# Kernel tuning notes

Measured on AMD Instinct MI355X. Metric: run time of the kernel, lower is better.

Reference implementation:

```python
import jax, jax.numpy as jnp
import numpy as np
import math

B, N, D, O, H = 8, 1024, 512, 512, 8
HD = O // H  # head_dim = 64


def setup_inputs() -> dict:
    key = jax.random.key(0)
    ks = jax.random.split(key, 12)
    x = jax.random.normal(ks[0], (B, N, D), dtype=jnp.float32)
    adj = jax.random.uniform(ks[1], (B, N, N), dtype=jnp.float32)  # unused by forward math
    mask = jax.random.randint(ks[2], (B, N), 0, 2) > 0  # bool padding mask
    # learned params (torch nn.Linear: y = x @ W.T + b)
    qkv_w = jax.random.normal(ks[3], (3 * O, D), dtype=jnp.float32) / math.sqrt(D)
    qkv_b = jnp.zeros((3 * O,), dtype=jnp.float32)
    # self_loop_W: 1/head_dim + U(0,1), per head, non-trainable
    self_loop_W = (1.0 / HD + jax.random.uniform(ks[4], (1, H, 1, 1))).astype(jnp.float32)
    w1 = jax.random.normal(ks[5], (O, O), dtype=jnp.float32) / math.sqrt(O)
    b1 = jnp.zeros((O,), dtype=jnp.float32)
    w2 = jax.random.normal(ks[6], (O, O), dtype=jnp.float32) / math.sqrt(O)
    b2 = jnp.zeros((O,), dtype=jnp.float32)
    wr = jax.random.normal(ks[7], (O, D), dtype=jnp.float32) / math.sqrt(D)
    br = jnp.zeros((O,), dtype=jnp.float32)
    return {"x": x, "adj": adj, "mask": mask, "self_loop_W": self_loop_W,
            "qkv_w": qkv_w, "qkv_b": qkv_b, "w1": w1, "b1": b1,
            "w2": w2, "b2": b2, "wr": wr, "br": br}


def reference(x, adj, mask, self_loop_W, qkv_w, qkv_b, w1, b1, w2, b2, wr, br):
    fmask = mask.astype(x.dtype)  # [B,N]
    # --- MoireAttention ---
    qkv = x @ qkv_w.T + qkv_b                       # [B,N,3O]
    qkv = qkv.reshape(B, N, 3, H, HD).transpose(2, 0, 3, 1, 4)  # [3,B,H,N,hd]
    Q, K, V = qkv[0], qkv[1], qkv[2]
    scores = jnp.einsum('bhnd,bhmd->bhnm', Q, K) / math.sqrt(HD)  # [B,H,N,N]
    eye = jnp.eye(N, dtype=scores.dtype)
    scores = scores + eye[None, None] * self_loop_W  # per-head diagonal self-loop bias
    mask2d = mask[:, None, :, None] & mask[:, None, None, :]  # [B,1,N,N]
    scores = jnp.where(mask2d, scores, jnp.asarray(-1e6, scores.dtype))
    attn = jax.nn.softmax(scores, axis=-1)
    h = jnp.einsum('bhnm,bhmd->bhnd', attn, V)      # [B,H,N,hd]
    h = h.transpose(0, 2, 1, 3).reshape(B, N, O)
    # --- mask, FFN (eval mode: noise/dropout are identity), mask ---
    h = h * fmask[..., None]
    h = jax.nn.relu(h @ w1.T + b1) @ w2.T + b2
    h = h * fmask[..., None]
    # --- residual blend ---
    x_proj = x @ wr.T + br
    return h * 0.5 + x_proj * 0.5
```

## Files before the change

### kernel.cpp

```cpp
#include <hip/hip_runtime.h>
#include <hip/hip_bf16.h>

typedef __attribute__((ext_vector_type(8))) short short8;
typedef __attribute__((ext_vector_type(4))) float f32x4;
typedef __attribute__((ext_vector_type(4))) short short4v;

#define BB 8
#define NN 1024
#define DD 512
#define OO 512
#define HH 8
#define HD 64
#define MM (BB * NN)

#define QSC 0.18033688f
#define KSHIFT -11.54156032f
#define KMASKED -30000.0f

__device__ __forceinline__ void gload_lds16(const void* g, void* l) {
  __builtin_amdgcn_global_load_lds(
      (const __attribute__((address_space(1))) void*)g,
      (__attribute__((address_space(3))) void*)l, 16, 0, 0);
}

__device__ __forceinline__ uint2 cvt4(float4 v) {
  union { uint2 u; __hip_bfloat16 h[4]; } t;
  t.h[0] = __float2bfloat16(v.x);
  t.h[1] = __float2bfloat16(v.y);
  t.h[2] = __float2bfloat16(v.z);
  t.h[3] = __float2bfloat16(v.w);
  return t.u;
}

#define SEG_N 10
struct ConvArgs {
  const float* src[SEG_N];
  __hip_bfloat16* dst[SEG_N];
  int n4[SEG_N];
};

__global__ void convert_kernel(ConvArgs a) {
  const int t = blockIdx.y;
  const int n4 = a.n4[t];
  const float4* fs = (const float4*)a.src[t];
  uint2* d = (uint2*)a.dst[t];
  for (int i = blockIdx.x * blockDim.x + threadIdx.x; i < n4;
       i += gridDim.x * blockDim.x)
    d[i] = cvt4(fs[i]);
}

__global__ __launch_bounds__(256) void gemm_qkv(
    const __hip_bfloat16* __restrict__ A0, const __hip_bfloat16* __restrict__ B0,
    const __hip_bfloat16* __restrict__ bias0, const __hip_bfloat16* __restrict__ bias1,
    __hip_bfloat16* __restrict__ out0, __hip_bfloat16* __restrict__ out1,
    __hip_bfloat16* __restrict__ out2, float* __restrict__ outf, int Kd) {
  __shared__ __align__(16) __hip_bfloat16 smem[16384];

  const int tid  = threadIdx.x;
  const int wave = tid >> 6;
  const int lane = tid & 63;
  const int fl   = lane & 15;
  const int fk   = (lane >> 4) * 8;
  const int wm   = (wave & 1) * 64;
  const int wn   = (wave >> 1) * 64;
  const int bid     = blockIdx.x;
  const int rowpart = 8 * (bid & 7) + ((bid >> 3) & 7);
  const int colpart = bid >> 6;
  const int m0 = rowpart * 128;
  const int n0 = colpart * 128;
  const int glr  = lane >> 2;
  const int glc  = (lane & 3) * 8;

  f32x4 acc[4][4];
#pragma unroll
  for (int i = 0; i < 4; ++i)
#pragma unroll
    for (int j = 0; j < 4; ++j) acc[i][j] = (f32x4){0.f, 0.f, 0.f, 0.f};

  char* lb = (char*)smem;
  for (int k0 = 0; k0 < Kd; k0 += 64) {
    __syncthreads();
    gload_lds16(A0 + (size_t)(m0 + wave * 16 + glr) * Kd + k0 + glc,
                lb + wave * 1024 + lane * 16);
    gload_lds16(A0 + (size_t)(m0 + 64 + wave * 16 + glr) * Kd + k0 + glc,
                lb + (wave + 4) * 1024 + lane * 16);
    gload_lds16(A0 + (size_t)(m0 + wave * 16 + glr) * Kd + k0 + 32 + glc,
                lb + 8192 + wave * 1024 + lane * 16);
    gload_lds16(A0 + (size_t)(m0 + 64 + wave * 16 + glr) * Kd + k0 + 32 + glc,
                lb + 8192 + (wave + 4) * 1024 + lane * 16);
    gload_lds16(B0 + (size_t)(n0 + wave * 16 + glr) * Kd + k0 + glc,
                lb + 16384 + wave * 1024 + lane * 16);
    gload_lds16(B0 + (size_t)(n0 + 64 + wave * 16 + glr) * Kd + k0 + glc,
                lb + 16384 + (wave + 4) * 1024 + lane * 16);
    gload_lds16(B0 + (size_t)(n0 + wave * 16 + glr) * Kd + k0 + 32 + glc,
                lb + 24576 + wave * 1024 + lane * 16);
    gload_lds16(B0 + (size_t)(n0 + 64 + wave * 16 + glr) * Kd + k0 + 32 + glc,
                lb + 24576 + (wave + 4) * 1024 + lane * 16);
    __syncthreads();

#pragma unroll
    for (int kh = 0; kh < 2; ++kh) {
      const __hip_bfloat16* Ap = smem + kh * 4096;
      const __hip_bfloat16* Bp = smem + 8192 + kh * 4096;
      short8 af[4], bfr[4];
#pragma unroll
      for (int i = 0; i < 4; ++i)
        af[i] = *(const short8*)&Ap[(wm + i * 16 + fl) * 32 + fk];
#pragma unroll
      for (int j = 0; j < 4; ++j)
        bfr[j] = *(const short8*)&Bp[(wn + j * 16 + fl) * 32 + fk];
#pragma unroll
      for (int i = 0; i < 4; ++i)
#pragma unroll
        for (int j = 0; j < 4; ++j)
          acc[i][j] = __builtin_amdgcn_mfma_f32_16x16x32_bf16(af[i], bfr[j],
                                                              acc[i][j], 0, 0, 0);
    }
  }

  const int rb = (lane >> 4) * 4;
  const int part = n0 >> 9;
  if (part < 2) {
    __hip_bfloat16* dst = (part == 0) ? out0 : out1;
    const float scf = (part == 0) ? QSC : 1.0f;
#pragma unroll
    for (int j = 0; j < 4; ++j) {
      const int colb  = n0 + wn + j * 16;
      const int o     = colb & 511;
      const int headq = o >> 6;
      const int d     = (o & 63) + fl;
      const float bi  = __bfloat162float(bias0[colb + fl]);
#pragma unroll
      for (int i = 0; i < 4; ++i) {
#pragma unroll
        for (int r = 0; r < 4; ++r) {
          const int row = m0 + wm + i * 16 + rb + r;
          const int bb  = row >> 10;
          const int nn  = row & 1023;
          dst[((size_t)((bb << 3) + headq) * NN + nn) * HD + d] =
              __float2bfloat16((acc[i][j][r] + bi) * scf);
        }
      }
    }
  } else if (part == 2) {
    __syncthreads();
    __hip_bfloat16* tsc = smem + wave * 1120;
    const int bb  = (m0 + wm) >> 10;
    const int nnb = (m0 + wm) & 1023;
    const int dl  = lane >> 2;
    const int cc  = (lane & 3) * 16;
#pragma unroll
    for (int j = 0; j < 4; ++j) {
      const int colb  = n0 + wn + j * 16;
      const int o     = colb & 511;
      const int headq = o >> 6;
      const int dbase = o & 63;
      const float bi  = __bfloat162float(bias0[colb + fl]);
#pragma unroll
      for (int i = 0; i < 4; ++i) {
#pragma unroll
        for (int r = 0; r < 4; ++r) {
          const int rr = i * 16 + rb + r;
          tsc[fl * 70 + rr] = __float2bfloat16(acc[i][j][r] + bi);
        }
      }
      uint4 r0 = *(const uint4*)&tsc[dl * 70 + cc];
      uint4 r1 = *(const uint4*)&tsc[dl * 70 + cc + 8];
      __hip_bfloat16* vdst =
          out2 + ((size_t)((bb << 3) + headq) * HD + dbase + dl) * NN + nnb;
      *(uint4*)&vdst[cc] = r0;
      *(uint4*)&vdst[cc + 8] = r1;
    }
  } else {
#pragma unroll
    for (int j = 0; j < 4; ++j) {
      const int colb = n0 + wn + j * 16;
      const int o    = colb & 511;
      const float bi = 0.5f * __bfloat162float(bias1[o + fl]);
#pragma unroll
      for (int i = 0; i < 4; ++i) {
#pragma unroll
        for (int r = 0; r < 4; ++r) {
          const int row = m0 + wm + i * 16 + rb + r;
          outf[(size_t)row * OO + o + fl] = 0.5f * acc[i][j][r] + bi;
        }
      }
    }
  }
}

__global__ __launch_bounds__(1024) void ffn_fused(
    const __hip_bfloat16* __restrict__ hb,
    const __hip_bfloat16* __restrict__ w1, const __hip_bfloat16* __restrict__ w2,
    const __hip_bfloat16* __restrict__ b1, const __hip_bfloat16* __restrict__ b2,
    const int* __restrict__ mask, float* __restrict__ outf) {
  __shared__ __align__(16) __hip_bfloat16 h1s[32 * 520];
  __shared__ float Mrow[32];

  const int tid  = threadIdx.x;
  const int wv   = tid >> 6;
  const int lane = tid & 63;
  const int fl   = lane & 15;
  const int quad = lane >> 4;
  const int fk   = quad * 8;
  const int m0   = blockIdx.x * 32;

  {
    const int col = (tid & 63) * 8;
#pragma unroll
    for (int c = 0; c < 2; ++c) {
      const int row = c * 16 + (tid >> 6);
      *(uint4*)&h1s[row * 520 + col] =
          *(const uint4*)&hb[(size_t)(m0 + row) * OO + col];
    }
    if (tid < 32) Mrow[tid] = (mask[m0 + tid] != 0) ? 1.f : 0.f;
  }
  __syncthreads();

  f32x4 acc[2][2];

  auto run_phase = [&](const __hip_bfloat16* __restrict__ W) {
    const __hip_bfloat16* wl0 = W + (size_t)(wv * 32 + fl) * 512 + fk;
    short8 a[6][2];
#pragma unroll
    for (int d = 0; d < 6; ++d)
#pragma unroll
      for (int j = 0; j < 2; ++j)
        a[d][j] = *(const short8*)(wl0 + d * 32 + j * 8192);
#pragma unroll
    for (int k = 0; k < 16; ++k) {
      short8 bh_[2];
#pragma unroll
      for (int i = 0; i < 2; ++i)
        bh_[i] = *(const short8*)&h1s[(i * 16 + fl) * 520 + k * 32 + fk];
      __builtin_amdgcn_s_setprio(1);
#pragma unroll
      for (int j = 0; j < 2; ++j)
#pragma unroll
        for (int i = 0; i < 2; ++i)
          acc[i][j] = __builtin_amdgcn_mfma_f32_16x16x32_bf16(a[k % 6][j], bh_[i],
                                                              acc[i][j], 0, 0, 0);
      __builtin_amdgcn_s_setprio(0);
      if (k < 10) {
#pragma unroll
        for (int j = 0; j < 2; ++j)
          a[k % 6][j] = *(const short8*)(wl0 + (k + 6) * 32 + j * 8192);
      }
      __builtin_amdgcn_sched_barrier(0);
    }
  };

#pragma unroll
  for (int i = 0; i < 2; ++i)
#pragma unroll
    for (int j = 0; j < 2; ++j) acc[i][j] = (f32x4){0.f, 0.f, 0.f, 0.f};
  run_phase(w1);
  __syncthreads();

#pragma unroll
  for (int j = 0; j < 2; ++j) {
    const int c0 = wv * 32 + j * 16 + quad * 4;
    union { short4v s; __hip_bfloat16 h[4]; } bv;
    bv.s = *(const short4v*)&b1[c0];
#pragma unroll
    for (int i = 0; i < 2; ++i) {
      const float mr = Mrow[i * 16 + fl];
      union { short4v s; __hip_bfloat16 h[4]; } pu;
#pragma unroll
      for (int e = 0; e < 4; ++e) {
        const float v = fmaxf(acc[i][j][e] + __bfloat162float(bv.h[e]), 0.f) * mr;
        pu.h[e] = __float2bfloat16(v);
      }
      *(short4v*)&h1s[(i * 16 + fl) * 520 + c0] = pu.s;
    }
  }
  __syncthreads();

#pragma unroll
  for (int i = 0; i < 2; ++i)
#pragma unroll
    for (int j = 0; j < 2; ++j) acc[i][j] = (f32x4){0.f, 0.f, 0.f, 0.f};
  run_phase(w2);

#pragma unroll
  for (int j = 0; j < 2; ++j) {
    const int c0 = wv * 32 + j * 16 + quad * 4;
    union { short4v s; __hip_bfloat16 h[4]; } b2v;
    b2v.s = *(const short4v*)&b2[c0];
#pragma unroll
    for (int i = 0; i < 2; ++i) {
      const float mr = Mrow[i * 16 + fl];
      const int row = m0 + i * 16 + fl;
      float4 prev = *(const float4*)&outf[(size_t)row * OO + c0];
      float4 o;
      o.x = prev.x + 0.5f * (acc[i][j][0] + mr * __bfloat162float(b2v.h[0]));
      o.y = prev.y + 0.5f * (acc[i][j][1] + mr * __bfloat162float(b2v.h[1]));
      o.z = prev.z + 0.5f * (acc[i][j][2] + mr * __bfloat162float(b2v.h[2]));
      o.w = prev.w + 0.5f * (acc[i][j][3] + mr * __bfloat162float(b2v.h[3]));
      *(float4*)&outf[(size_t)row * OO + c0] = o;
    }
  }
}

__global__ __launch_bounds__(512) void attn_kernel(
    const __hip_bfloat16* __restrict__ Qb, const __hip_bfloat16* __restrict__ Kb,
    const __hip_bfloat16* __restrict__ Vt, const __hip_bfloat16* __restrict__ slw,
    const int* __restrict__ mask, __hip_bfloat16* __restrict__ hb) {
  __shared__ __align__(16) __hip_bfloat16 QPs[256 * 72];
  __shared__ __align__(16) __hip_bfloat16 Ks[2][64 * 72];
  __shared__ __align__(16) __hip_bfloat16 Vs[2][64 * 72];
  __shared__ float Msf[NN];

  const int tid  = threadIdx.x;
  const int wave = tid >> 6;
  const int lane = tid & 63;
  const int fl   = lane & 15;
  const int quad = lane >> 4;
  const int fk   = quad * 8;
  const int rb   = quad * 4;
  const int bh   = blockIdx.x & 63;
  const int qblk = blockIdx.x >> 6;
  const int b    = bh >> 3;
  const int head = bh & 7;
  const int q0   = qblk * 256;

  const float slwL2 = __bfloat162float(slw[head]) * 1.44269504f;

  const int twf  = 2 * wave;
  const int kbdA = 4 * qblk + (twf >> 2);
  const int jdA  = twf & 3;
  const int kbdB = 4 * qblk + ((twf + 1) >> 2);
  const int jdB  = (twf + 1) & 3;

  const int srow2 = tid >> 3;
  const int sc2   = (tid & 7) * 8;
  const __hip_bfloat16* kgb = Kb + (size_t)bh * NN * HD;
  const __hip_bfloat16* vgb = Vt + (size_t)bh * HD * NN;

  uint4 kr = *(const uint4*)(kgb + (size_t)srow2 * HD + sc2);
  uint4 vr = *(const uint4*)(vgb + (size_t)srow2 * NN + sc2);
  {
    const int qr = tid >> 1;
    const int qc = (tid & 1) * 32;
    const __hip_bfloat16* qg = Qb + ((size_t)bh * NN + q0 + qr) * HD + qc;
    uint4 v0 = *(const uint4*)(qg);
    uint4 v1 = *(const uint4*)(qg + 8);
    uint4 v2 = *(const uint4*)(qg + 16);
    uint4 v3 = *(const uint4*)(qg + 24);
    *(uint4*)&QPs[qr * 72 + qc] = v0;
    *(uint4*)&QPs[qr * 72 + qc + 8] = v1;
    *(uint4*)&QPs[qr * 72 + qc + 16] = v2;
    *(uint4*)&QPs[qr * 72 + qc + 24] = v3;
#pragma unroll
    for (int k = 0; k < 2; ++k) {
      const int idx = tid * 2 + k;
      Msf[idx] = (mask[b * NN + idx] != 0) ? KSHIFT : KMASKED;
    }
  }
  *(uint4*)&Ks[0][srow2 * 72 + sc2] = kr;
  *(uint4*)&Vs[0][srow2 * 72 + sc2] = vr;
  kr = *(const uint4*)(kgb + (size_t)(64 + srow2) * HD + sc2);
  vr = *(const uint4*)(vgb + (size_t)srow2 * NN + 64 + sc2);
  __syncthreads();
  const short8 qa0A = *(const short8*)&QPs[(wave * 32 + fl) * 72 + fk];
  const short8 qa1A = *(const short8*)&QPs[(wave * 32 + fl) * 72 + fk + 32];
  const short8 qa0B = *(const short8*)&QPs[(wave * 32 + 16 + fl) * 72 + fk];
  const short8 qa1B = *(const short8*)&QPs[(wave * 32 + 16 + fl) * 72 + fk + 32];

  float lsumA = 0.f, lsumB = 0.f;
  f32x4 OaccA[4], OaccB[4];
#pragma unroll
  for (int t = 0; t < 4; ++t) {
    OaccA[t] = (f32x4){0.f, 0.f, 0.f, 0.f};
    OaccB[t] = (f32x4){0.f, 0.f, 0.f, 0.f};
  }

  for (int kb = 0; kb < NN / 64; ++kb) {
    const int kbase = kb * 64;
    const int cur   = kb & 1;
    const __hip_bfloat16* Kc = Ks[cur];
    const __hip_bfloat16* Vc = Vs[cur];

    f32x4 sfrA[4], sfrB[4];
    __builtin_amdgcn_s_setprio(1);
#pragma unroll
    for (int j = 0; j < 4; ++j) {
      const short8 kf0 = *(const short8*)&Kc[(j * 16 + fl) * 72 + fk];
      const short8 kf1 = *(const short8*)&Kc[(j * 16 + fl) * 72 + fk + 32];
      f32x4 zA = (f32x4){0.f, 0.f, 0.f, 0.f};
      zA = __builtin_amdgcn_mfma_f32_16x16x32_bf16(kf0, qa0A, zA, 0, 0, 0);
      zA = __builtin_amdgcn_mfma_f32_16x16x32_bf16(kf1, qa1A, zA, 0, 0, 0);
      sfrA[j] = zA;
      f32x4 zB = (f32x4){0.f, 0.f, 0.f, 0.f};
      zB = __builtin_amdgcn_mfma_f32_16x16x32_bf16(kf0, qa0B, zB, 0, 0, 0);
      zB = __builtin_amdgcn_mfma_f32_16x16x32_bf16(kf1, qa1B, zB, 0, 0, 0);
      sfrB[j] = zB;
    }
    __builtin_amdgcn_s_setprio(0);

    if ((fl >> 2) == quad && (kb == kbdA || kb == kbdB)) {
#pragma unroll
      for (int j = 0; j < 4; ++j)
#pragma unroll
        for (int e = 0; e < 4; ++e)
          if ((fl & 3) == e) {
            if (kb == kbdA && j == jdA) sfrA[j][e] += slwL2;
            if (kb == kbdB && j == jdB) sfrB[j][e] += slwL2;
          }
    }

#pragma unroll
    for (int j = 0; j < 4; ++j) {
      const f32x4 mb4 = *(const f32x4*)&Msf[kbase + j * 16 + quad * 4];
      union { short4v s; __hip_bfloat16 h[4]; } puA, puB;
      float psA = 0.f, psB = 0.f;
#pragma unroll
      for (int e = 0; e < 4; ++e) {
        const float pvA = exp2f(sfrA[j][e] + mb4[e]);
        psA += pvA;
        puA.h[e] = __float2bfloat16(pvA);
        const float pvB = exp2f(sfrB[j][e] + mb4[e]);
        psB += pvB;
        puB.h[e] = __float2bfloat16(pvB);
      }
      lsumA += psA;
      lsumB += psB;
      *(short4v*)&QPs[(wave * 32 + fl) * 72 + j * 16 + quad * 4] = puA.s;
      *(short4v*)&QPs[(wave * 32 + 16 + fl) * 72 + j * 16 + quad * 4] = puB.s;
    }

    const short8 paA0 = *(const short8*)&QPs[(wave * 32 + fl) * 72 + fk];
    const short8 paA1 = *(const short8*)&QPs[(wave * 32 + fl) * 72 + fk + 32];
    const short8 paB0 = *(const short8*)&QPs[(wave * 32 + 16 + fl) * 72 + fk];
    const short8 paB1 = *(const short8*)&QPs[(wave * 32 + 16 + fl) * 72 + fk + 32];
    __builtin_amdgcn_s_setprio(1);
#pragma unroll
    for (int t = 0; t < 4; ++t) {
      const short8 vf0 = *(const short8*)&Vc[(t * 16 + fl) * 72 + fk];
      const short8 vf1 = *(const short8*)&Vc[(t * 16 + fl) * 72 + fk + 32];
      OaccA[t] = __builtin_amdgcn_mfma_f32_16x16x32_bf16(paA0, vf0, OaccA[t], 0, 0, 0);
      OaccA[t] = __builtin_amdgcn_mfma_f32_16x16x32_bf16(paA1, vf1, OaccA[t], 0, 0, 0);
      OaccB[t] = __builtin_amdgcn_mfma_f32_16x16x32_bf16(paB0, vf0, OaccB[t], 0, 0, 0);
      OaccB[t] = __builtin_amdgcn_mfma_f32_16x16x32_bf16(paB1, vf1, OaccB[t], 0, 0, 0);
    }
    __builtin_amdgcn_s_setprio(0);

    if (kb + 1 < NN / 64) {
      *(uint4*)&Ks[cur ^ 1][srow2 * 72 + sc2] = kr;
      *(uint4*)&Vs[cur ^ 1][srow2 * 72 + sc2] = vr;
      if (kb + 2 < NN / 64) {
        const int nk = kbase + 128;
        kr = *(const uint4*)(kgb + (size_t)(nk + srow2) * HD + sc2);
        vr = *(const uint4*)(vgb + (size_t)srow2 * NN + nk + sc2);
      }
      __builtin_amdgcn_sched_barrier(0);
      __syncthreads();
    }
  }

#pragma unroll
  for (int f = 0; f < 2; ++f) {
    float l = (f == 0) ? lsumA : lsumB;
    l += __shfl_xor(l, 16, 64);
    l += __shfl_xor(l, 32, 64);
    const int qrow_me = q0 + wave * 32 + f * 16 + fl;
    const float qm = (mask[b * NN + qrow_me] != 0) ? 1.f : 0.f;
    const float sf = qm / fmaxf(l, 1e-30f);
    float scl[4];
#pragma unroll
    for (int r = 0; r < 4; ++r) scl[r] = __shfl(sf, rb + r, 64);
#pragma unroll
    for (int t = 0; t < 4; ++t) {
      const int d = t * 16 + fl;
#pragma unroll
      for (int r = 0; r < 4; ++r) {
        const int qrow_g = q0 + wave * 32 + f * 16 + rb + r;
        const float ov = (f == 0) ? OaccA[t][r] : OaccB[t][r];
        hb[(size_t)(b * NN + qrow_g) * OO + head * HD + d] =
            __float2bfloat16(ov * scl[r]);
      }
    }
  }
}

extern "C" void kernel_launch(void* const* d_in, const int* in_sizes, int n_in,
                              void* d_out, int out_size, void* d_ws, size_t ws_size,
                              hipStream_t stream) {
  const float* x_raw    = (const float*)d_in[0];
  const int* mask       = (const int*)d_in[2];
  const float* slw_raw  = (const float*)d_in[3];
  const float* qkvw_raw = (const float*)d_in[4];
  const float* qkvb_raw = (const float*)d_in[5];
  const float* w1_raw   = (const float*)d_in[6];
  const float* b1_raw   = (const float*)d_in[7];
  const float* w2_raw   = (const float*)d_in[8];
  const float* b2_raw   = (const float*)d_in[9];
  const float* wr_raw   = (const float*)d_in[10];
  const float* br_raw   = (const float*)d_in[11];
  float* outf           = (float*)d_out;

  __hip_bfloat16* p = (__hip_bfloat16*)d_ws;
  __hip_bfloat16* xc    = p; p += (size_t)MM * DD;
  __hip_bfloat16* qkvwc = p; p += 3 * OO * DD;
  __hip_bfloat16* wrc   = p; p += OO * DD;
  __hip_bfloat16* w1c   = p; p += OO * OO;
  __hip_bfloat16* w2c   = p; p += OO * OO;
  __hip_bfloat16* qkvbc = p; p += 3 * OO;
  __hip_bfloat16* b1c   = p; p += OO;
  __hip_bfloat16* b2c   = p; p += OO;
  __hip_bfloat16* brc   = p; p += OO;
  __hip_bfloat16* slwc  = p; p += 64;
  const size_t ebuf = (size_t)BB * HH * NN * HD;
  __hip_bfloat16* Qb = p; p += ebuf;
  __hip_bfloat16* Kb = p; p += ebuf;
  __hip_bfloat16* Vb = p; p += ebuf;
  __hip_bfloat16* hb = p; p += ebuf;

  if (ws_size < (size_t)((char*)p - (char*)d_ws)) return;

  ConvArgs ca;
  ca.src[0] = x_raw;    ca.dst[0] = xc;    ca.n4[0] = MM * DD / 4;
  ca.src[1] = qkvw_raw; ca.dst[1] = qkvwc; ca.n4[1] = 3 * OO * DD / 4;
  ca.src[2] = w1_raw;   ca.dst[2] = w1c;   ca.n4[2] = OO * OO / 4;
  ca.src[3] = w2_raw;   ca.dst[3] = w2c;   ca.n4[3] = OO * OO / 4;
  ca.src[4] = wr_raw;   ca.dst[4] = wrc;   ca.n4[4] = OO * DD / 4;
  ca.src[5] = qkvb_raw; ca.dst[5] = qkvbc; ca.n4[5] = 3 * OO / 4;
  ca.src[6] = b1_raw;   ca.dst[6] = b1c;   ca.n4[6] = OO / 4;
  ca.src[7] = b2_raw;   ca.dst[7] = b2c;   ca.n4[7] = OO / 4;
  ca.src[8] = br_raw;   ca.dst[8] = brc;   ca.n4[8] = OO / 4;
  ca.src[9] = slw_raw;  ca.dst[9] = slwc;  ca.n4[9] = HH / 4;
  convert_kernel<<<dim3(1024, SEG_N), 256, 0, stream>>>(ca);

  gemm_qkv<<<1024, 256, 0, stream>>>(xc, qkvwc, qkvbc, brc, Qb, Kb, Vb, outf, DD);
  attn_kernel<<<BB * HH * (NN / 256), 512, 0, stream>>>(Qb, Kb, Vb, slwc, mask, hb);
  ffn_fused<<<256, 1024, 0, stream>>>(hb, w1c, w2c, b1c, b2c, mask, outf);
}
```

Measured before the change: 206.0 us.

## Software-pipeline attention loop: overlap next QK MFMA with current PV and softmax

Splits the attention inner loop into QK, softmax and PV stages and reorders them so each iteration issues the QK MFMAs for the next key tile before the PV MFMAs of the current one. Softmax then runs on the freshly computed scores. This is meant to interleave the MFMA work with the exp/convert work and hide latency. The K/V LDS staging grows from double to triple buffering so V of the current tile stays live while the next tile is loaded. That raises LDS use per block, which could cut occupancy if more than one block would otherwise share a CU.

```diff
diff --git a/kernel.cpp b/kernel.cpp
--- a/kernel.cpp
+++ b/kernel.cpp
@@ -307,8 +307,8 @@
     const __hip_bfloat16* __restrict__ Vt, const __hip_bfloat16* __restrict__ slw,
     const int* __restrict__ mask, __hip_bfloat16* __restrict__ hb) {
   __shared__ __align__(16) __hip_bfloat16 QPs[256 * 72];
-  __shared__ __align__(16) __hip_bfloat16 Ks[2][64 * 72];
-  __shared__ __align__(16) __hip_bfloat16 Vs[2][64 * 72];
+  __shared__ __align__(16) __hip_bfloat16 Ks[3][64 * 72];
+  __shared__ __align__(16) __hip_bfloat16 Vs[3][64 * 72];
   __shared__ float Msf[NN];
 
   const int tid  = threadIdx.x;
@@ -375,13 +375,9 @@
     OaccB[t] = (f32x4){0.f, 0.f, 0.f, 0.f};
   }
 
-  for (int kb = 0; kb < NN / 64; ++kb) {
-    const int kbase = kb * 64;
-    const int cur   = kb & 1;
-    const __hip_bfloat16* Kc = Ks[cur];
-    const __hip_bfloat16* Vc = Vs[cur];
-
-    f32x4 sfrA[4], sfrB[4];
+  f32x4 sfrA[4], sfrB[4];
+
+  auto qk_tile = [&](const __hip_bfloat16* Kc) {
     __builtin_amdgcn_s_setprio(1);
 #pragma unroll
     for (int j = 0; j < 4; ++j) {
@@ -397,18 +393,20 @@
       sfrB[j] = zB;
     }
     __builtin_amdgcn_s_setprio(0);
-
-    if ((fl >> 2) == quad && (kb == kbdA || kb == kbdB)) {
+  };
+
+  auto softmax_tile = [&](int kb2) {
+    if ((fl >> 2) == quad && (kb2 == kbdA || kb2 == kbdB)) {
 #pragma unroll
       for (int j = 0; j < 4; ++j)
 #pragma unroll
         for (int e = 0; e < 4; ++e)
           if ((fl & 3) == e) {
-            if (kb == kbdA && j == jdA) sfrA[j][e] += slwL2;
-            if (kb == kbdB && j == jdB) sfrB[j][e] += slwL2;
+            if (kb2 == kbdA && j == jdA) sfrA[j][e] += slwL2;
+            if (kb2 == kbdB && j == jdB) sfrB[j][e] += slwL2;
           }
     }
-
+    const int kbase = kb2 * 64;
 #pragma unroll
     for (int j = 0; j < 4; ++j) {
       const f32x4 mb4 = *(const f32x4*)&Msf[kbase + j * 16 + quad * 4];
@@ -428,7 +426,9 @@
       *(short4v*)&QPs[(wave * 32 + fl) * 72 + j * 16 + quad * 4] = puA.s;
       *(short4v*)&QPs[(wave * 32 + 16 + fl) * 72 + j * 16 + quad * 4] = puB.s;
     }
-
+  };
+
+  auto pv_tile = [&](const __hip_bfloat16* Vc) {
     const short8 paA0 = *(const short8*)&QPs[(wave * 32 + fl) * 72 + fk];
     const short8 paA1 = *(const short8*)&QPs[(wave * 32 + fl) * 72 + fk + 32];
     const short8 paB0 = *(const short8*)&QPs[(wave * 32 + 16 + fl) * 72 + fk];
@@ -444,19 +444,29 @@
       OaccB[t] = __builtin_amdgcn_mfma_f32_16x16x32_bf16(paB1, vf1, OaccB[t], 0, 0, 0);
     }
     __builtin_amdgcn_s_setprio(0);
-
-    if (kb + 1 < NN / 64) {
-      *(uint4*)&Ks[cur ^ 1][srow2 * 72 + sc2] = kr;
-      *(uint4*)&Vs[cur ^ 1][srow2 * 72 + sc2] = vr;
-      if (kb + 2 < NN / 64) {
-        const int nk = kbase + 128;
-        kr = *(const uint4*)(kgb + (size_t)(nk + srow2) * HD + sc2);
-        vr = *(const uint4*)(vgb + (size_t)srow2 * NN + nk + sc2);
-      }
-      __builtin_amdgcn_sched_barrier(0);
-      __syncthreads();
-    }
-  }
+  };
+
+  qk_tile(Ks[0]);
+  softmax_tile(0);
+
+  for (int kb = 0; kb < NN / 64 - 1; ++kb) {
+    const int nxt = kb + 1;
+    const int nb  = nxt % 3;
+    *(uint4*)&Ks[nb][srow2 * 72 + sc2] = kr;
+    *(uint4*)&Vs[nb][srow2 * 72 + sc2] = vr;
+    if (kb + 2 < NN / 64) {
+      const int nk = (kb + 2) * 64;
+      kr = *(const uint4*)(kgb + (size_t)(nk + srow2) * HD + sc2);
+      vr = *(const uint4*)(vgb + (size_t)srow2 * NN + nk + sc2);
+    }
+    __builtin_amdgcn_sched_barrier(0);
+    __syncthreads();
+
+    qk_tile(Ks[nb]);
+    pv_tile(Vs[kb % 3]);
+    softmax_tile(nxt);
+  }
+  pv_tile(Vs[(NN / 64 - 1) % 3]);
 
 #pragma unroll
   for (int f = 0; f < 2; ++f) {
```

After: 205.9 us. No clear change (-0.1%).
